# Performance work log

Hardware: AMD Instinct MI355X
Metric: run time of the kernel (lower is better)

Reference implementation:

```python
import jax, jax.numpy as jnp
import numpy as np


def setup_inputs() -> dict:
    key = jax.random.key(0)
    kq, kk, kv = jax.random.split(key, 3)
    B, H, S, D = 2, 8, 4096, 64
    return {
        "query": jax.random.normal(kq, (B, H, S, D), dtype=jnp.float32),
        "key": jax.random.normal(kk, (B, H, S, D), dtype=jnp.float32),
        "value": jax.random.normal(kv, (B, H, S, D), dtype=jnp.float32),
    }


def reference(query, key, value):
    # NOTE: the torch source overwrites sqrt(d) with d, so the divisor is D, not sqrt(D).
    d = query.shape[-1]
    # score: [B, H, S_q, S_k]
    score = jnp.einsum("bhqd,bhkd->bhqk", query, key) / d
    relu = jax.nn.relu(score)  # no softmax / row normalization
    out = jnp.einsum("bhqk,bhkd->bhqd", relu, value)
    return out
```

## Files before the change

kernel.cpp:

```cpp
#include <hip/hip_runtime.h>
#include <hip/hip_bf16.h>
#include <stdint.h>


#define NH 16
#define SEQ 4096
#define DD 64
#define HE (SEQ*DD)
#define HB (HE*2)
#define Q16_OFF 0
#define K16_OFF (NH*HB)
#define V16_OFF (2*NH*HB)
#define WS_NEED (3*NH*HB)

typedef __attribute__((ext_vector_type(8)))  short    bf16x8;
typedef __attribute__((ext_vector_type(16))) float    f32x16;
typedef __attribute__((ext_vector_type(4)))  uint32_t u32x4;

__device__ inline uint32_t f2bf1(float f) {
  return (uint32_t)__builtin_bit_cast(unsigned short, __float2bfloat16(f));
}
__device__ inline uint32_t pack2bf(float a, float b) {
  return f2bf1(a) | (f2bf1(b) << 16);
}
__device__ inline uint32_t cvtpk(float lo, float hi) {
  uint32_t r;
  asm("v_cvt_pk_bf16_f32 %0, %1, %2" : "=v"(r) : "v"(lo), "v"(hi));
  return r;
}
__device__ inline uint32_t relu2(uint32_t w) {
  uint32_t r;
  asm("v_pk_max_f16 %0, %1, 0" : "=v"(r) : "v"(w));
  return r;
}

__global__ __launch_bounds__(256) void prepass_kernel(const float* __restrict__ Q,
                                                      const float* __restrict__ K,
                                                      const float* __restrict__ V,
                                                      char* __restrict__ ws) {
  __shared__ float vt[64*65];
  int bx = blockIdx.x, tid = threadIdx.x;
  if (bx < 2048) {
    int head = bx >> 7, qg = bx & 127;
    int r31 = tid & 31, c = tid >> 5;
    const float4* s = (const float4*)(Q + (size_t)head*HE + ((size_t)(qg*32 + r31))*64 + c*8);
    float4 a = s[0], b = s[1];
    const float sc = 1.0f/64.0f;
    u32x4 o;
    o.x = pack2bf(a.x*sc, a.y*sc);
    o.y = pack2bf(a.z*sc, a.w*sc);
    o.z = pack2bf(b.x*sc, b.y*sc);
    o.w = pack2bf(b.z*sc, b.w*sc);
    char* tb = ws + Q16_OFF + (size_t)head*HB;
    *(u32x4*)(tb + ((qg*4 + (c >> 1))*1024) + ((c & 1)*32 + r31)*16) = o;
  } else if (bx < 3072) {
    int tile = bx - 2048;
    int head = tile >> 6, t = tile & 63;
    int r = tid >> 2, c0 = (tid & 3) * 16;
    const float4* s4 = (const float4*)(K + (size_t)head*HE + ((size_t)(t*64 + r))*64 + c0);
    float4 f0 = s4[0], f1 = s4[1], f2 = s4[2], f3 = s4[3];
    u32x4 c_lo, c_hi;
    c_lo.x = pack2bf(f0.x, f0.y); c_lo.y = pack2bf(f0.z, f0.w);
    c_lo.z = pack2bf(f1.x, f1.y); c_lo.w = pack2bf(f1.z, f1.w);
    c_hi.x = pack2bf(f2.x, f2.y); c_hi.y = pack2bf(f2.z, f2.w);
    c_hi.z = pack2bf(f3.x, f3.y); c_hi.w = pack2bf(f3.z, f3.w);
    char* tb = ws + K16_OFF + ((size_t)head*64 + t)*8192;
    char* chunk = tb + ((r >> 5)*4 + (tid & 3))*1024 + (r & 31)*16;
    *(u32x4*)(chunk)       = c_lo;
    *(u32x4*)(chunk + 512) = c_hi;
  } else {
    int tile = bx - 3072;
    int head = tile >> 6, t = tile & 63;
    int k = tid >> 2, c0 = (tid & 3)*16;
    const float4* s4 = (const float4*)(V + (size_t)head*HE + ((size_t)(t*64 + k))*64 + c0);
    float4 f0 = s4[0], f1 = s4[1], f2 = s4[2], f3 = s4[3];
    float tmp[16] = {f0.x,f0.y,f0.z,f0.w, f1.x,f1.y,f1.z,f1.w,
                     f2.x,f2.y,f2.z,f2.w, f3.x,f3.y,f3.z,f3.w};
    #pragma unroll
    for (int j = 0; j < 16; ++j) vt[k*65 + c0 + j] = tmp[j];
    __syncthreads();
    int d = tid >> 2, k0 = (tid & 3)*16;
    float v2[16];
    #pragma unroll
    for (int j = 0; j < 16; ++j) v2[j] = vt[(k0 + j)*65 + d];
    u32x4 c_lo, c_hi;
    c_lo.x = pack2bf(v2[0],  v2[1]);  c_lo.y = pack2bf(v2[2],  v2[3]);
    c_lo.z = pack2bf(v2[4],  v2[5]);  c_lo.w = pack2bf(v2[6],  v2[7]);
    c_hi.x = pack2bf(v2[8],  v2[9]);  c_hi.y = pack2bf(v2[10], v2[11]);
    c_hi.z = pack2bf(v2[12], v2[13]); c_hi.w = pack2bf(v2[14], v2[15]);
    char* tb = ws + V16_OFF + ((size_t)head*64 + t)*8192;
    char* chunk = tb + ((d >> 5)*4 + (tid & 3))*1024 + (d & 31)*16;
    *(u32x4*)(chunk)       = c_lo;
    *(u32x4*)(chunk + 512) = c_hi;
  }
}

__global__ __launch_bounds__(256, 2) void attn_kernel(const char* __restrict__ ws,
                                                      float* __restrict__ out) {
  __shared__ __align__(16) char lds[6*8192];
  int bid = blockIdx.x;
  int bx = (bid & 7) * 64 + (bid >> 3);
  int head = bx >> 5, qblk = bx & 31;
  int tid = threadIdx.x;
  int lane = tid & 63, w = tid >> 6;
  int l31 = lane & 31, h = lane >> 5;
  int g  = w >> 1;
  int wg = w & 1;

  const char* q16   = ws + Q16_OFF + (size_t)head*HB;
  const char* kbase = ws + K16_OFF + (size_t)head*HB + (size_t)g*32*8192;
  const char* vbase = ws + V16_OFF + (size_t)head*HB + (size_t)g*32*8192;

  int qg0 = qblk*4 + wg*2;
  bf16x8 qf[2][4];
  #pragma unroll
  for (int m = 0; m < 2; ++m)
    #pragma unroll
    for (int t = 0; t < 4; ++t)
      qf[m][t] = *(const bf16x8*)(q16 + ((size_t)((qg0 + m)*4 + t))*1024 + lane*16);

  f32x16 kZero;
  #pragma unroll
  for (int i = 0; i < 16; ++i) kZero[i] = 0.f;

  f32x16 o[2][2];
  #pragma unroll
  for (int m = 0; m < 2; ++m)
    #pragma unroll
    for (int nd = 0; nd < 2; ++nd)
      #pragma unroll
      for (int i = 0; i < 16; ++i) o[m][nd][i] = 0.f;

  bf16x8 vf[2][4];

  auto stageK = [&](int kt) {
    const char* ktile = kbase + (size_t)kt*8192;
    char* lk = lds + (size_t)(g*3 + kt % 3)*8192;
    #pragma unroll
    for (int c = 0; c < 4; ++c) {
      int off = (wg*4 + c)*1024;
      __builtin_amdgcn_global_load_lds(
          (const __attribute__((address_space(1))) void*)(ktile + off + lane*16),
          (__attribute__((address_space(3))) void*)(lk + off), 16, 0, 0);
    }
  };
  auto loadV = [&](int kt) {
    const char* vp = vbase + (size_t)kt*8192;
    #pragma unroll
    for (int i = 0; i < 8; ++i)
      vf[i >> 2][i & 3] = *(const bf16x8*)(vp + i*1024 + lane*16);
  };

  stageK(0);
  stageK(1);
  #pragma unroll 1
  for (int kt = 0; kt < 32; ++kt) {
    if (kt >= 30) asm volatile("s_waitcnt vmcnt(0)" ::: "memory");
    else          asm volatile("s_waitcnt vmcnt(4)" ::: "memory");
    __builtin_amdgcn_s_barrier();

    loadV(kt);
    if (kt + 2 < 32) stageK(kt + 2);

    const char* lk = lds + (size_t)(g*3 + kt % 3)*8192;
    bf16x8 kf[2][4];
    #pragma unroll
    for (int i = 0; i < 8; ++i)
      kf[i >> 2][i & 3] = *(const bf16x8*)(lk + i*1024 + lane*16);

    f32x16 st[2][2];
    #pragma unroll
    for (int n = 0; n < 2; ++n) {
      __builtin_amdgcn_s_setprio(1);
      #pragma unroll
      for (int m = 0; m < 2; ++m) {
        f32x16 acc = __builtin_amdgcn_mfma_f32_32x32x16_bf16(kf[n][0], qf[m][0], kZero, 0, 0, 0);
        #pragma unroll
        for (int t = 1; t < 4; ++t)
          acc = __builtin_amdgcn_mfma_f32_32x32x16_bf16(kf[n][t], qf[m][t], acc, 0, 0, 0);
        st[m][n] = acc;
      }
      __builtin_amdgcn_s_setprio(0);
    }

    bf16x8 pa[2][4];
    #pragma unroll
    for (int m = 0; m < 2; ++m)
      #pragma unroll
      for (int n = 0; n < 2; ++n)
        #pragma unroll
        for (int kn = 0; kn < 2; ++kn) {
          uint32_t w0 = cvtpk(st[m][n][kn*8+0], st[m][n][kn*8+1]);
          uint32_t w1 = cvtpk(st[m][n][kn*8+2], st[m][n][kn*8+3]);
          uint32_t w2 = cvtpk(st[m][n][kn*8+4], st[m][n][kn*8+5]);
          uint32_t w3 = cvtpk(st[m][n][kn*8+6], st[m][n][kn*8+7]);
          asm("v_permlane32_swap_b32 %0, %1" : "+v"(w0), "+v"(w2));
          asm("v_permlane32_swap_b32 %0, %1" : "+v"(w1), "+v"(w3));
          union { uint32_t u[4]; bf16x8 v; } pk;
          pk.u[0] = relu2(w0);
          pk.u[1] = relu2(w1);
          pk.u[2] = relu2(w2);
          pk.u[3] = relu2(w3);
          pa[m][n*2 + kn] = pk.v;
        }

    __builtin_amdgcn_s_setprio(1);
    #pragma unroll
    for (int m = 0; m < 2; ++m)
      #pragma unroll
      for (int nd = 0; nd < 2; ++nd)
        #pragma unroll
        for (int ks = 0; ks < 4; ++ks)
          o[m][nd] = __builtin_amdgcn_mfma_f32_32x32x16_bf16(pa[m][ks], vf[nd][ks], o[m][nd], 0, 0, 0);
    __builtin_amdgcn_s_setprio(0);
  }

  __syncthreads();
  float* red = (float*)lds;
  if (g == 1) {
    #pragma unroll
    for (int m = 0; m < 2; ++m)
      #pragma unroll
      for (int nd = 0; nd < 2; ++nd)
        #pragma unroll
        for (int r = 0; r < 16; ++r) {
          int ql = wg*64 + m*32 + (r & 3) + 8*(r >> 2) + 4*h;
          red[ql*64 + nd*32 + l31] = o[m][nd][r];
        }
  }
  __syncthreads();
  if (g == 0) {
    float* outh = out + (size_t)head*HE;
    #pragma unroll
    for (int m = 0; m < 2; ++m)
      #pragma unroll
      for (int nd = 0; nd < 2; ++nd)
        #pragma unroll
        for (int r = 0; r < 16; ++r) {
          int ql = wg*64 + m*32 + (r & 3) + 8*(r >> 2) + 4*h;
          float v = o[m][nd][r] + red[ql*64 + nd*32 + l31];
          outh[(size_t)(qblk*128 + ql)*64 + nd*32 + l31] = v;
        }
  }
}

extern "C" void kernel_launch(void* const* d_in, const int* in_sizes, int n_in,
                              void* d_out, int out_size, void* d_ws, size_t ws_size,
                              hipStream_t stream) {
  if (n_in < 3 || ws_size < (size_t)WS_NEED) return;
  const float* Q = (const float*)d_in[0];
  const float* K = (const float*)d_in[1];
  const float* V = (const float*)d_in[2];
  float* out = (float*)d_out;
  char* ws = (char*)d_ws;
  hipLaunchKernelGGL(prepass_kernel, dim3(4096), dim3(256), 0, stream, Q, K, V, ws);
  hipLaunchKernelGGL(attn_kernel,    dim3(512),  dim3(256), 0, stream, ws, out);
}
```

Measured before the change: 82.27 us.

## Stage V through LDS with K, double-buffer, and interleave relu packing with PV MFMAs

```diff
diff --git a/kernel.cpp b/kernel.cpp
--- a/kernel.cpp
+++ b/kernel.cpp
@@ -97,7 +97,7 @@
 
 __global__ __launch_bounds__(256, 2) void attn_kernel(const char* __restrict__ ws,
                                                       float* __restrict__ out) {
-  __shared__ __align__(16) char lds[6*8192];
+  __shared__ __align__(16) char lds[2*2*16384];
   int bid = blockIdx.x;
   int bx = (bid & 7) * 64 + (bid >> 3);
   int head = bx >> 5, qblk = bx & 31;
@@ -131,87 +131,98 @@
       #pragma unroll
       for (int i = 0; i < 16; ++i) o[m][nd][i] = 0.f;
 
-  bf16x8 vf[2][4];
-
-  auto stageK = [&](int kt) {
+  auto stage = [&](int kt) {
     const char* ktile = kbase + (size_t)kt*8192;
-    char* lk = lds + (size_t)(g*3 + kt % 3)*8192;
+    const char* vtile = vbase + (size_t)kt*8192;
+    char* lk = lds + (size_t)(g*2 + (kt & 1))*16384;
+    char* lv = lk + 8192;
     #pragma unroll
     for (int c = 0; c < 4; ++c) {
       int off = (wg*4 + c)*1024;
       __builtin_amdgcn_global_load_lds(
           (const __attribute__((address_space(1))) void*)(ktile + off + lane*16),
           (__attribute__((address_space(3))) void*)(lk + off), 16, 0, 0);
+      __builtin_amdgcn_global_load_lds(
+          (const __attribute__((address_space(1))) void*)(vtile + off + lane*16),
+          (__attribute__((address_space(3))) void*)(lv + off), 16, 0, 0);
     }
   };
-  auto loadV = [&](int kt) {
-    const char* vp = vbase + (size_t)kt*8192;
-    #pragma unroll
-    for (int i = 0; i < 8; ++i)
-      vf[i >> 2][i & 3] = *(const bf16x8*)(vp + i*1024 + lane*16);
-  };
-
-  stageK(0);
-  stageK(1);
+
+  stage(0);
   #pragma unroll 1
   for (int kt = 0; kt < 32; ++kt) {
-    if (kt >= 30) asm volatile("s_waitcnt vmcnt(0)" ::: "memory");
-    else          asm volatile("s_waitcnt vmcnt(4)" ::: "memory");
+    asm volatile("s_waitcnt vmcnt(0)" ::: "memory");
     __builtin_amdgcn_s_barrier();
-
-    loadV(kt);
-    if (kt + 2 < 32) stageK(kt + 2);
-
-    const char* lk = lds + (size_t)(g*3 + kt % 3)*8192;
+    if (kt + 1 < 32) stage(kt + 1);
+
+    const char* lk = lds + (size_t)(g*2 + (kt & 1))*16384;
+    const char* lv = lk + 8192;
+
     bf16x8 kf[2][4];
     #pragma unroll
     for (int i = 0; i < 8; ++i)
       kf[i >> 2][i & 3] = *(const bf16x8*)(lk + i*1024 + lane*16);
 
     f32x16 st[2][2];
-    #pragma unroll
-    for (int n = 0; n < 2; ++n) {
-      __builtin_amdgcn_s_setprio(1);
+    __builtin_amdgcn_s_setprio(1);
+    #pragma unroll
+    for (int n = 0; n < 2; ++n)
+      #pragma unroll
+      for (int m = 0; m < 2; ++m)
+        st[m][n] = __builtin_amdgcn_mfma_f32_32x32x16_bf16(kf[n][0], qf[m][0], kZero, 0, 0, 0);
+    #pragma unroll
+    for (int t = 1; t < 4; ++t)
+      #pragma unroll
+      for (int n = 0; n < 2; ++n)
+        #pragma unroll
+        for (int m = 0; m < 2; ++m)
+          st[m][n] = __builtin_amdgcn_mfma_f32_32x32x16_bf16(kf[n][t], qf[m][t], st[m][n], 0, 0, 0);
+    __builtin_amdgcn_s_setprio(0);
+
+    bf16x8 vf[2][4];
+    #pragma unroll
+    for (int i = 0; i < 8; ++i)
+      vf[i >> 2][i & 3] = *(const bf16x8*)(lv + i*1024 + lane*16);
+
+    bf16x8 pa[2][4];
+    auto packg = [&](int n, int kn) {
       #pragma unroll
       for (int m = 0; m < 2; ++m) {
-        f32x16 acc = __builtin_amdgcn_mfma_f32_32x32x16_bf16(kf[n][0], qf[m][0], kZero, 0, 0, 0);
-        #pragma unroll
-        for (int t = 1; t < 4; ++t)
-          acc = __builtin_amdgcn_mfma_f32_32x32x16_bf16(kf[n][t], qf[m][t], acc, 0, 0, 0);
-        st[m][n] = acc;
+        uint32_t w0 = cvtpk(st[m][n][kn*8+0], st[m][n][kn*8+1]);
+        uint32_t w1 = cvtpk(st[m][n][kn*8+2], st[m][n][kn*8+3]);
+        uint32_t w2 = cvtpk(st[m][n][kn*8+4], st[m][n][kn*8+5]);
+        uint32_t w3 = cvtpk(st[m][n][kn*8+6], st[m][n][kn*8+7]);
+        asm("v_permlane32_swap_b32 %0, %1" : "+v"(w0), "+v"(w2));
+        asm("v_permlane32_swap_b32 %0, %1" : "+v"(w1), "+v"(w3));
+        union { uint32_t u[4]; bf16x8 v; } pk;
+        pk.u[0] = relu2(w0);
+        pk.u[1] = relu2(w1);
+        pk.u[2] = relu2(w2);
+        pk.u[3] = relu2(w3);
+        pa[m][n*2 + kn] = pk.v;
       }
-      __builtin_amdgcn_s_setprio(0);
-    }
-
-    bf16x8 pa[2][4];
-    #pragma unroll
-    for (int m = 0; m < 2; ++m)
-      #pragma unroll
-      for (int n = 0; n < 2; ++n)
-        #pragma unroll
-        for (int kn = 0; kn < 2; ++kn) {
-          uint32_t w0 = cvtpk(st[m][n][kn*8+0], st[m][n][kn*8+1]);
-          uint32_t w1 = cvtpk(st[m][n][kn*8+2], st[m][n][kn*8+3]);
-          uint32_t w2 = cvtpk(st[m][n][kn*8+4], st[m][n][kn*8+5]);
-          uint32_t w3 = cvtpk(st[m][n][kn*8+6], st[m][n][kn*8+7]);
-          asm("v_permlane32_swap_b32 %0, %1" : "+v"(w0), "+v"(w2));
-          asm("v_permlane32_swap_b32 %0, %1" : "+v"(w1), "+v"(w3));
-          union { uint32_t u[4]; bf16x8 v; } pk;
-          pk.u[0] = relu2(w0);
-          pk.u[1] = relu2(w1);
-          pk.u[2] = relu2(w2);
-          pk.u[3] = relu2(w3);
-          pa[m][n*2 + kn] = pk.v;
-        }
-
-    __builtin_amdgcn_s_setprio(1);
-    #pragma unroll
-    for (int m = 0; m < 2; ++m)
-      #pragma unroll
-      for (int nd = 0; nd < 2; ++nd)
-        #pragma unroll
-        for (int ks = 0; ks < 4; ++ks)
+    };
+    auto pvks = [&](int ks) {
+      #pragma unroll
+      for (int m = 0; m < 2; ++m)
+        #pragma unroll
+        for (int nd = 0; nd < 2; ++nd)
           o[m][nd] = __builtin_amdgcn_mfma_f32_32x32x16_bf16(pa[m][ks], vf[nd][ks], o[m][nd], 0, 0, 0);
+    };
+
+    packg(0, 0);
+    packg(0, 1);
+    __builtin_amdgcn_s_setprio(1);
+    pvks(0);
+    __builtin_amdgcn_s_setprio(0);
+    packg(1, 0);
+    __builtin_amdgcn_s_setprio(1);
+    pvks(1);
+    __builtin_amdgcn_s_setprio(0);
+    packg(1, 1);
+    __builtin_amdgcn_s_setprio(1);
+    pvks(2);
+    pvks(3);
     __builtin_amdgcn_s_setprio(0);
   }
 
```

Result: faster. 78.94 us (-4.1%).
